# Performance work log

Hardware: AMD Instinct MI355X
Metric: run time of the kernel (lower is better)

The kernel has to match this reference:

```python
import jax, jax.numpy as jnp
import numpy as np

RADIUS = 0.2
NSAMPLE = 32
EPS = 1e-5  # BatchNorm2d default eps


def _bn_relu(x, g, b):
    # BatchNorm2d in training mode: per-channel stats over (B, S, nsample), biased var.
    m = x.mean(axis=(0, 1, 2))
    v = jnp.mean((x - m) ** 2, axis=(0, 1, 2))
    return jax.nn.relu((x - m) * jax.lax.rsqrt(v + EPS) * g + b)


def setup_inputs() -> dict:
    key = jax.random.key(0)
    ks = jax.random.split(key, 8)
    B, N, S = 8, 8192, 2048
    xyz = jax.random.uniform(ks[0], (B, 3, N), dtype=jnp.float32)          # unit cube
    points = jax.random.normal(ks[1], (B, 3, N), dtype=jnp.float32)
    fps_idx = jax.random.randint(ks[2], (B, S), 0, N, dtype=jnp.int32)
    W1 = jax.random.normal(ks[3], (64, 6), dtype=jnp.float32) * 0.1
    W2 = jax.random.normal(ks[4], (64, 64), dtype=jnp.float32) * 0.1
    W3 = jax.random.normal(ks[5], (128, 64), dtype=jnp.float32) * 0.1
    return dict(
        xyz=xyz, points=points, fps_idx=fps_idx,
        W1=W1, g1=jnp.ones((64,)), b1=jnp.zeros((64,)),
        W2=W2, g2=jnp.ones((64,)), b2=jnp.zeros((64,)),
        W3=W3, g3=jnp.ones((128,)), b3=jnp.zeros((128,)),
    )


def reference(xyz, points, fps_idx, W1, g1, b1, W2, g2, b2, W3, g3, b3):
    B, _, N = xyz.shape
    xyz_t = jnp.transpose(xyz, (0, 2, 1))            # [B,N,3]
    pts_t = jnp.transpose(points, (0, 2, 1))         # [B,N,D]
    # gather_operation: sampled centers
    new_xyz_t = jnp.take_along_axis(xyz_t, fps_idx[:, :, None], axis=1)  # [B,S,3]
    # ball query: first NSAMPLE points within radius; pad with first hit
    d2 = jnp.sum((new_xyz_t[:, :, None, :] - xyz_t[:, None, :, :]) ** 2, axis=-1)  # [B,S,N]
    keys = jnp.where(d2 <= RADIUS * RADIUS, jnp.arange(N, dtype=jnp.int32), N)
    neg_top, _ = jax.lax.top_k(-keys, NSAMPLE)       # smallest keys first
    idx = -neg_top                                   # [B,S,NSAMPLE]
    idx = jnp.where(idx < N, idx, idx[:, :, 0:1])    # pad empty slots with first hit (self always in-radius)
    bidx = jnp.arange(B)[:, None, None]
    grouped_xyz = xyz_t[bidx, idx]                   # [B,S,ns,3]
    rel = grouped_xyz - new_xyz_t[:, :, None, :]     # center-relative coords
    grouped_pts = pts_t[bidx, idx]                   # [B,S,ns,D]
    feat = jnp.concatenate([rel, grouped_pts], axis=-1)  # [B,S,ns,3+D]
    for W, g, b in ((W1, g1, b1), (W2, g2, b2), (W3, g3, b3)):
        feat = _bn_relu(jnp.einsum('bsnc,oc->bsno', feat, W), g, b)
    new_points = jnp.max(feat, axis=2)               # max over neighbors -> [B,S,C]
    return jnp.transpose(new_xyz_t, (0, 2, 1)), jnp.transpose(new_points, (0, 2, 1))
```

## Files before the change

### kernel.cpp

```cpp
#include <hip/hip_runtime.h>
#include <hip/hip_bf16.h>

#define BB_ 8
#define NN_ 8192
#define SS_ 2048
#define NS 32
#define C1 64
#define C2 64
#define C3 128
#define RAD2 0.04f
#define BN_EPS 1e-5f
#define M_TOT (BB_*SS_*NS)

typedef __attribute__((ext_vector_type(8))) short bf16x8;
typedef __attribute__((ext_vector_type(4))) float f32x4;

#define FBF_OFF 0
#define WPK_OFF 2097152
#define ST_OFF  2104320
#define AFF_OFF 2104832
#define GMM_OFF 2105344

__device__ inline unsigned pkbf(float a, float b) {
    __hip_bfloat162 h = __float22bfloat162_rn(make_float2(a, b));
    unsigned r; __builtin_memcpy(&r, &h, 4); return r;
}
__device__ inline bf16x8 asfrag(uint4 v) { bf16x8 r; __builtin_memcpy(&r, &v, 16); return r; }
__device__ inline float bflo(unsigned u) { unsigned x = u << 16; float f; __builtin_memcpy(&f, &x, 4); return f; }
__device__ inline float bfhi(unsigned u) { unsigned x = u & 0xffff0000u; float f; __builtin_memcpy(&f, &x, 4); return f; }

__global__ void k_zero(float* __restrict__ st) { st[threadIdx.x] = 0.f; }

__global__ void k_ballquery(const float* __restrict__ xyz, const float* __restrict__ pts,
                            const int* __restrict__ fps, uint4* __restrict__ fbf) {
    __shared__ int lidx[4][NS];
    int wave = (blockIdx.x * blockDim.x + threadIdx.x) >> 6;
    int lane = threadIdx.x & 63;
    int wslot = threadIdx.x >> 6;
    int b = wave / SS_;
    const float* xb = xyz + (size_t)b * 3 * NN_;
    const float* pb = pts + (size_t)b * 3 * NN_;
    int ci = fps[wave];
    float cx = xb[ci], cy = xb[NN_ + ci], cz = xb[2 * NN_ + ci];

    int found = 0;
    int first_i = -1;
    for (int base = 0; base < NN_; base += 64) {
        int i = base + lane;
        float dx = xb[i] - cx, dy = xb[NN_ + i] - cy, dz = xb[2 * NN_ + i] - cz;
        float d2 = __fadd_rn(__fadd_rn(__fmul_rn(dx, dx), __fmul_rn(dy, dy)), __fmul_rn(dz, dz));
        bool inr = d2 <= RAD2;
        unsigned long long mask = __ballot(inr);
        if (first_i < 0 && mask) first_i = base + __builtin_ctzll(mask);
        if (inr) {
            int pos = found + __popcll(mask & ((1ull << lane) - 1ull));
            if (pos < NS) lidx[wslot][pos] = i;
        }
        found += __popcll(mask);
        if (found >= NS) break;
    }
    if (found > NS) found = NS;
    __syncthreads();

    if (lane < NS) {
        int j = (lane < found) ? lidx[wslot][lane] : first_i;
        uint4 o;
        o.x = pkbf(xb[j] - cx,           xb[NN_ + j] - cy);
        o.y = pkbf(xb[2 * NN_ + j] - cz, pb[j]);
        o.z = pkbf(pb[NN_ + j],          pb[2 * NN_ + j]);
        o.w = 0u;
        fbf[(size_t)wave * NS + lane] = o;
    }
}

__global__ void k_xyz(const float* __restrict__ xyz, const int* __restrict__ fps,
                      float* __restrict__ out_xyz) {
    int t = blockIdx.x * 256 + threadIdx.x;
    if (t >= BB_ * 3 * SS_) return;
    int b = t / (3 * SS_);
    int r = (t / SS_) % 3;
    int s = t % SS_;
    int ci = fps[b * SS_ + s];
    out_xyz[t] = xyz[((size_t)b * 3 + r) * NN_ + ci];
}

__global__ void k_pack(const float* __restrict__ W1, const float* __restrict__ W2,
                       const float* __restrict__ W3, uint4* __restrict__ wf) {
    int t = blockIdx.x * 256 + threadIdx.x;
    if (t >= 1792) return;
    int l = t & 63, p = l & 15, qd = l >> 4;
    float v[8];
    if (t < 256) {
        int mt = t >> 6;
        #pragma unroll
        for (int j = 0; j < 8; ++j)
            v[j] = (qd == 0 && j < 6) ? W1[(mt * 16 + p) * 6 + j] : 0.f;
    } else if (t < 768) {
        int fr = (t - 256) >> 6;
        int mt = fr >> 1, kf = fr & 1;
        #pragma unroll
        for (int j = 0; j < 8; ++j)
            v[j] = W2[(16 * mt + p) * 64 + kf * 32 + qd * 8 + j];
    } else {
        int fr = (t - 768) >> 6;
        int nt = fr >> 1, kf = fr & 1;
        #pragma unroll
        for (int j = 0; j < 8; ++j)
            v[j] = W3[(nt * 16 + p) * 64 + kf * 32 + qd * 8 + j];
    }
    uint4 o;
    o.x = pkbf(v[0], v[1]); o.y = pkbf(v[2], v[3]);
    o.z = pkbf(v[4], v[5]); o.w = pkbf(v[6], v[7]);
    wf[t] = o;
}

__global__ void k_p1(const uint4* __restrict__ fbf, float* __restrict__ st) {
    __shared__ float sacc[27];
    int tid = threadIdx.x;
    if (tid < 27) sacc[tid] = 0.f;
    __syncthreads();
    int gt = blockIdx.x * 256 + tid;
    float vals[27];
    #pragma unroll
    for (int i = 0; i < 27; ++i) vals[i] = 0.f;
    #pragma unroll 1
    for (int it = 0; it < M_TOT / 16384; ++it) {
        uint4 w = fbf[it * 16384 + gt];
        float f[6] = { bflo(w.x), bfhi(w.x), bflo(w.y), bfhi(w.y), bflo(w.z), bfhi(w.z) };
        #pragma unroll
        for (int c = 0; c < 6; ++c) vals[c] += f[c];
        int q = 6;
        #pragma unroll
        for (int c = 0; c < 6; ++c)
            #pragma unroll
            for (int d = c; d < 6; ++d) { vals[q] = fmaf(f[c], f[d], vals[q]); ++q; }
    }
    int lane = tid & 63;
    #pragma unroll
    for (int i = 0; i < 27; ++i) {
        float v = vals[i];
        #pragma unroll
        for (int d = 32; d; d >>= 1) v += __shfl_xor(v, d);
        if (lane == 0) atomicAdd(&sacc[i], v);
    }
    __syncthreads();
    if (tid < 27) atomicAdd(&st[tid], sacc[tid]);
}

__global__ void k_fin1(const float* __restrict__ st, const float* __restrict__ W1,
                       const float* __restrict__ g, const float* __restrict__ bb,
                       float* __restrict__ a, float* __restrict__ c) {
    int o = threadIdx.x;
    if (o >= C1) return;
    float w[6];
    #pragma unroll
    for (int i = 0; i < 6; ++i) w[i] = W1[o * 6 + i];
    float ms = 0.f;
    #pragma unroll
    for (int i = 0; i < 6; ++i) ms = fmaf(w[i], st[i], ms);
    float m = ms / (float)M_TOT;
    float e2 = 0.f;
    #pragma unroll
    for (int ci = 0; ci < 6; ++ci)
        #pragma unroll
        for (int d = 0; d < 6; ++d) {
            int lo = ci < d ? ci : d, hi = ci < d ? d : ci;
            int idx = 6 + lo * 6 - lo * (lo + 1) / 2 + hi;
            e2 = fmaf(w[ci] * w[d], st[idx], e2);
        }
    float var = e2 / (float)M_TOT - m * m;
    float ai = g[o] * (1.0f / sqrtf(var + BN_EPS));
    a[o] = ai;
    c[o] = bb[o] - m * ai;
}

__global__ void k_fin(const float* __restrict__ gsum, const float* __restrict__ gsq,
                      const float* __restrict__ g, const float* __restrict__ bb,
                      float* __restrict__ a, float* __restrict__ c, int C) {
    int t = threadIdx.x;
    if (t < C) {
        float m = gsum[t] / (float)M_TOT;
        float var = gsq[t] / (float)M_TOT - m * m;
        float ai = g[t] * (1.0f / sqrtf(var + BN_EPS));
        a[t] = ai;
        c[t] = bb[t] - m * ai;
    }
}

__global__ __launch_bounds__(256) void k_p2(
        const uint4* __restrict__ fbf, const uint4* __restrict__ wpk,
        const float* __restrict__ aff,
        float* __restrict__ gsum, float* __restrict__ gsq) {
    __shared__ unsigned yls[4][2560];
    __shared__ float bs[C2], bq[C2];
    int tid = threadIdx.x, wslot = tid >> 6, lane = tid & 63;
    int p = lane & 15, qd = lane >> 4;
    if (tid < C2) { bs[tid] = 0.f; bq[tid] = 0.f; }
    __syncthreads();
    const float* a1 = aff, *c1 = aff + 64;
    const uint4* w1f = wpk;
    const uint4* w2f = wpk + 256;
    unsigned* my = yls[wslot];
    float s2[4][4], q2[4][4];
    #pragma unroll
    for (int i = 0; i < 4; ++i)
        #pragma unroll
        for (int r = 0; r < 4; ++r) { s2[i][r] = 0.f; q2[i][r] = 0.f; }

    #pragma unroll 1
    for (int it = 0; it < 4; ++it) {
        int tile = it * 2048 + blockIdx.x * 4 + wslot;
        int base = tile * 64;
        bf16x8 B1[4];
        #pragma unroll
        for (int nt = 0; nt < 4; ++nt) {
            uint4 v = make_uint4(0u, 0u, 0u, 0u);
            if (qd == 0) v = fbf[base + nt * 16 + p];
            B1[nt] = asfrag(v);
        }
        #pragma unroll
        for (int mt = 0; mt < 4; ++mt) {
            bf16x8 A = asfrag(w1f[mt * 64 + lane]);
            float4 av = *(const float4*)(a1 + mt * 16 + qd * 4);
            float4 cv = *(const float4*)(c1 + mt * 16 + qd * 4);
            #pragma unroll
            for (int nt = 0; nt < 4; ++nt) {
                f32x4 acc = {0.f, 0.f, 0.f, 0.f};
                acc = __builtin_amdgcn_mfma_f32_16x16x32_bf16(A, B1[nt], acc, 0, 0, 0);
                float y0 = fmaxf(fmaf(av.x, acc[0], cv.x), 0.f);
                float y1 = fmaxf(fmaf(av.y, acc[1], cv.y), 0.f);
                float y2 = fmaxf(fmaf(av.z, acc[2], cv.z), 0.f);
                float y3 = fmaxf(fmaf(av.w, acc[3], cv.w), 0.f);
                int a = (nt * 16 + p) * 40 + mt * 8 + qd * 2;
                *(uint2*)&my[a] = make_uint2(pkbf(y0, y1), pkbf(y2, y3));
            }
        }
        __syncthreads();
        bf16x8 B2[4][2];
        #pragma unroll
        for (int nt = 0; nt < 4; ++nt)
            #pragma unroll
            for (int kf = 0; kf < 2; ++kf)
                B2[nt][kf] = asfrag(*(const uint4*)&my[(nt * 16 + p) * 40 + kf * 16 + qd * 4]);
        #pragma unroll
        for (int mt = 0; mt < 4; ++mt) {
            f32x4 acc[4];
            #pragma unroll
            for (int nt = 0; nt < 4; ++nt) acc[nt] = (f32x4){0.f, 0.f, 0.f, 0.f};
            #pragma unroll
            for (int kf = 0; kf < 2; ++kf) {
                bf16x8 W = asfrag(w2f[(mt * 2 + kf) * 64 + lane]);
                #pragma unroll
                for (int nt = 0; nt < 4; ++nt)
                    acc[nt] = __builtin_amdgcn_mfma_f32_16x16x32_bf16(W, B2[nt][kf], acc[nt], 0, 0, 0);
            }
            #pragma unroll
            for (int r = 0; r < 4; ++r) {
                float v0 = acc[0][r], v1 = acc[1][r], v2 = acc[2][r], v3 = acc[3][r];
                s2[mt][r] += (v0 + v1) + (v2 + v3);
                q2[mt][r] = fmaf(v0, v0, fmaf(v1, v1, fmaf(v2, v2, fmaf(v3, v3, q2[mt][r]))));
            }
        }
        __syncthreads();
    }
    #pragma unroll
    for (int mt = 0; mt < 4; ++mt)
        #pragma unroll
        for (int r = 0; r < 4; ++r) {
            float s = s2[mt][r], q = q2[mt][r];
            #pragma unroll
            for (int off = 1; off <= 8; off <<= 1) { s += __shfl_xor(s, off); q += __shfl_xor(q, off); }
            if (p == 0) {
                atomicAdd(&bs[mt * 16 + qd * 4 + r], s);
                atomicAdd(&bq[mt * 16 + qd * 4 + r], q);
            }
        }
    __syncthreads();
    if (tid < C2) { atomicAdd(&gsum[tid], bs[tid]); atomicAdd(&gsq[tid], bq[tid]); }
}

__global__ __launch_bounds__(256) void k_p3(
        const uint4* __restrict__ fbf, const uint4* __restrict__ wpk,
        const float* __restrict__ aff,
        float* __restrict__ gsum, float* __restrict__ gsq, float2* __restrict__ gmm) {
    __shared__ unsigned yls[4][2560];
    __shared__ float bs[C3], bq[C3];
    int tid = threadIdx.x, wslot = tid >> 6, lane = tid & 63;
    int p = lane & 15, qd = lane >> 4;
    if (tid < 128) bs[tid] = 0.f; else bq[tid - 128] = 0.f;
    __syncthreads();
    const float* a1 = aff, *c1 = aff + 64, *a2 = aff + 128, *c2 = aff + 192;
    const uint4* w1f = wpk;
    const uint4* w2f = wpk + 256;
    const uint4* w3f = wpk + 768;
    unsigned* my = yls[wslot];
    bf16x8 W3f[8][2];
    #pragma unroll
    for (int nt = 0; nt < 8; ++nt)
        #pragma unroll
        for (int kf = 0; kf < 2; ++kf)
            W3f[nt][kf] = asfrag(w3f[(nt * 2 + kf) * 64 + lane]);
    float gs3[8], gq3[8];
    #pragma unroll
    for (int i = 0; i < 8; ++i) { gs3[i] = 0.f; gq3[i] = 0.f; }

    #pragma unroll 1
    for (int it = 0; it < 4; ++it) {
        int tile = it * 2048 + blockIdx.x * 4 + wslot;
        int base = tile * 64;
        bf16x8 B1[4];
        #pragma unroll
        for (int nt = 0; nt < 4; ++nt) {
            uint4 v = make_uint4(0u, 0u, 0u, 0u);
            if (qd == 0) v = fbf[base + nt * 16 + p];
            B1[nt] = asfrag(v);
        }
        #pragma unroll
        for (int mt = 0; mt < 4; ++mt) {
            bf16x8 A = asfrag(w1f[mt * 64 + lane]);
            float4 av = *(const float4*)(a1 + mt * 16 + qd * 4);
            float4 cv = *(const float4*)(c1 + mt * 16 + qd * 4);
            #pragma unroll
            for (int nt = 0; nt < 4; ++nt) {
                f32x4 acc = {0.f, 0.f, 0.f, 0.f};
                acc = __builtin_amdgcn_mfma_f32_16x16x32_bf16(A, B1[nt], acc, 0, 0, 0);
                float y0 = fmaxf(fmaf(av.x, acc[0], cv.x), 0.f);
                float y1 = fmaxf(fmaf(av.y, acc[1], cv.y), 0.f);
                float y2 = fmaxf(fmaf(av.z, acc[2], cv.z), 0.f);
                float y3 = fmaxf(fmaf(av.w, acc[3], cv.w), 0.f);
                int a = (nt * 16 + p) * 40 + mt * 8 + qd * 2;
                *(uint2*)&my[a] = make_uint2(pkbf(y0, y1), pkbf(y2, y3));
            }
        }
        __syncthreads();
        bf16x8 B2[4][2];
        #pragma unroll
        for (int nt = 0; nt < 4; ++nt)
            #pragma unroll
            for (int kf = 0; kf < 2; ++kf)
                B2[nt][kf] = asfrag(*(const uint4*)&my[(nt * 16 + p) * 40 + kf * 16 + qd * 4]);
        __syncthreads();
        #pragma unroll
        for (int mt = 0; mt < 4; ++mt) {
            f32x4 acc[4];
            #pragma unroll
            for (int nt = 0; nt < 4; ++nt) acc[nt] = (f32x4){0.f, 0.f, 0.f, 0.f};
            #pragma unroll
            for (int kf = 0; kf < 2; ++kf) {
                bf16x8 W = asfrag(w2f[(mt * 2 + kf) * 64 + lane]);
                #pragma unroll
                for (int nt = 0; nt < 4; ++nt)
                    acc[nt] = __builtin_amdgcn_mfma_f32_16x16x32_bf16(W, B2[nt][kf], acc[nt], 0, 0, 0);
            }
            float4 av = *(const float4*)(a2 + mt * 16 + qd * 4);
            float4 cv = *(const float4*)(c2 + mt * 16 + qd * 4);
            #pragma unroll
            for (int nt = 0; nt < 4; ++nt) {
                float y0 = fmaxf(fmaf(av.x, acc[nt][0], cv.x), 0.f);
                float y1 = fmaxf(fmaf(av.y, acc[nt][1], cv.y), 0.f);
                float y2 = fmaxf(fmaf(av.z, acc[nt][2], cv.z), 0.f);
                float y3 = fmaxf(fmaf(av.w, acc[nt][3], cv.w), 0.f);
                int a = (nt * 16 + p) * 40 + mt * 8 + qd * 2;
                *(uint2*)&my[a] = make_uint2(pkbf(y0, y1), pkbf(y2, y3));
            }
        }
        __syncthreads();
        float gmx[2][8], gmn[2][8];
        #pragma unroll
        for (int mt = 0; mt < 4; ++mt) {
            bf16x8 A0 = asfrag(*(const uint4*)&my[(mt * 16 + p) * 40 + qd * 4]);
            bf16x8 A1 = asfrag(*(const uint4*)&my[(mt * 16 + p) * 40 + 16 + qd * 4]);
            f32x4 acc[8];
            #pragma unroll
            for (int nt = 0; nt < 8; ++nt) {
                acc[nt] = __builtin_amdgcn_mfma_f32_16x16x32_bf16(A0, W3f[nt][0],
                            (f32x4){0.f, 0.f, 0.f, 0.f}, 0, 0, 0);
                acc[nt] = __builtin_amdgcn_mfma_f32_16x16x32_bf16(A1, W3f[nt][1], acc[nt], 0, 0, 0);
            }
            int gh = mt >> 1;
            #pragma unroll
            for (int nt = 0; nt < 8; ++nt) {
                float v0 = acc[nt][0], v1 = acc[nt][1], v2 = acc[nt][2], v3 = acc[nt][3];
                gs3[nt] += (v0 + v1) + (v2 + v3);
                gq3[nt] = fmaf(v0, v0, fmaf(v1, v1, fmaf(v2, v2, fmaf(v3, v3, gq3[nt]))));
                float mx = fmaxf(fmaxf(v0, v1), fmaxf(v2, v3));
                float mn = fminf(fminf(v0, v1), fminf(v2, v3));
                if ((mt & 1) == 0) { gmx[gh][nt] = mx; gmn[gh][nt] = mn; }
                else { gmx[gh][nt] = fmaxf(gmx[gh][nt], mx); gmn[gh][nt] = fminf(gmn[gh][nt], mn); }
            }
        }
        #pragma unroll
        for (int grp = 0; grp < 2; ++grp)
            #pragma unroll
            for (int nt = 0; nt < 8; ++nt) {
                float mx = gmx[grp][nt], mn = gmn[grp][nt];
                mx = fmaxf(mx, __shfl_xor(mx, 16)); mx = fmaxf(mx, __shfl_xor(mx, 32));
                mn = fminf(mn, __shfl_xor(mn, 16)); mn = fminf(mn, __shfl_xor(mn, 32));
                if (lane < 16)
                    gmm[(size_t)(tile * 2 + grp) * C3 + nt * 16 + lane] = make_float2(mx, mn);
            }
        __syncthreads();
    }
    #pragma unroll
    for (int nt = 0; nt < 8; ++nt) {
        float s = gs3[nt], q = gq3[nt];
        s += __shfl_xor(s, 16); s += __shfl_xor(s, 32);
        q += __shfl_xor(q, 16); q += __shfl_xor(q, 32);
        if (lane < 16) {
            atomicAdd(&bs[nt * 16 + lane], s);
            atomicAdd(&bq[nt * 16 + lane], q);
        }
    }
    __syncthreads();
    if (tid < C3) { atomicAdd(&gsum[tid], bs[tid]); atomicAdd(&gsq[tid], bq[tid]); }
}

__global__ void k_out(const float2* __restrict__ gmm, const float* __restrict__ a3,
                      const float* __restrict__ c3, float* __restrict__ outp) {
    int s = blockIdx.x * 256 + threadIdx.x;
    int o = blockIdx.y, b = blockIdx.z;
    float2 mm = gmm[((size_t)(b * SS_ + s)) * C3 + o];
    float a = a3[o], c = c3[o];
    float v = (a >= 0.f) ? mm.x : mm.y;
    outp[((size_t)b * C3 + o) * SS_ + s] = fmaxf(fmaf(a, v, c), 0.f);
}

extern "C" void kernel_launch(void* const* d_in, const int* in_sizes, int n_in,
                              void* d_out, int out_size, void* d_ws, size_t ws_size,
                              hipStream_t stream) {
    (void)in_sizes; (void)n_in; (void)out_size; (void)ws_size;
    const float* xyz = (const float*)d_in[0];
    const float* pts = (const float*)d_in[1];
    const int*   fps = (const int*)d_in[2];
    const float* W1 = (const float*)d_in[3];
    const float* g1 = (const float*)d_in[4];
    const float* b1 = (const float*)d_in[5];
    const float* W2 = (const float*)d_in[6];
    const float* g2 = (const float*)d_in[7];
    const float* b2 = (const float*)d_in[8];
    const float* W3 = (const float*)d_in[9];
    const float* g3 = (const float*)d_in[10];
    const float* b3 = (const float*)d_in[11];
    float* out = (float*)d_out;
    float* ws = (float*)d_ws;

    uint4* fbf = (uint4*)(ws + FBF_OFF);
    uint4* wpk = (uint4*)(ws + WPK_OFF);
    float* st  = ws + ST_OFF;
    float* sum2 = st + 64,  *sq2 = st + 128;
    float* sum3 = st + 192, *sq3 = st + 320;
    float* af = ws + AFF_OFF;
    float* a1 = af,       *c1 = af + 64;
    float* a2 = af + 128, *c2 = af + 192;
    float* a3 = af + 256, *c3 = af + 384;
    float2* gmm = (float2*)(ws + GMM_OFF);

    k_zero<<<1, 512, 0, stream>>>(st);
    k_pack<<<7, 256, 0, stream>>>(W1, W2, W3, wpk);
    k_ballquery<<<(BB_ * SS_) / 4, 256, 0, stream>>>(xyz, pts, fps, fbf);
    k_p1<<<64, 256, 0, stream>>>(fbf, st);
    k_fin1<<<1, 64, 0, stream>>>(st, W1, g1, b1, a1, c1);
    k_p2<<<512, 256, 0, stream>>>(fbf, wpk, af, sum2, sq2);
    k_fin<<<1, 128, 0, stream>>>(sum2, sq2, g2, b2, a2, c2, C2);
    k_p3<<<512, 256, 0, stream>>>(fbf, wpk, af, sum3, sq3, gmm);
    k_fin<<<1, 128, 0, stream>>>(sum3, sq3, g3, b3, a3, c3, C3);
    k_out<<<dim3(SS_ / 256, C3, BB_), 256, 0, stream>>>(gmm, a3, c3,
                                                        out + (size_t)BB_ * 3 * SS_);
    k_xyz<<<(BB_ * 3 * SS_ + 255) / 256, 256, 0, stream>>>(xyz, fps, out);
}
```

Before: 247.5 us.

## Merge small kernels, stage W3 in LDS, store single max, coalesce output

Folds the stats zeroing into the weight-pack kernel and the xyz gather into a new output kernel that transposes through shared memory for coalesced float4 stores. The conv kernels now use doubled grids with launch_bounds occupancy hints, a YSTR=34 LDS row stride, and wave-local fences in place of block barriers. Layer 3 keeps W3 in LDS instead of registers and picks max or negated min by the sign of g3 inside the kernel, storing one float per channel instead of a max/min pair. The aim is fewer launches, less register pressure, less global traffic and fewer LDS bank conflicts. The risks are extra LDS reads for W3 and reliance on wave-private LDS buffers for correctness.

```diff
diff --git a/kernel.cpp b/kernel.cpp
--- a/kernel.cpp
+++ b/kernel.cpp
@@ -11,6 +11,7 @@
 #define RAD2 0.04f
 #define BN_EPS 1e-5f
 #define M_TOT (BB_*SS_*NS)
+#define YSTR 34
 
 typedef __attribute__((ext_vector_type(8))) short bf16x8;
 typedef __attribute__((ext_vector_type(4))) float f32x4;
@@ -28,8 +29,6 @@
 __device__ inline bf16x8 asfrag(uint4 v) { bf16x8 r; __builtin_memcpy(&r, &v, 16); return r; }
 __device__ inline float bflo(unsigned u) { unsigned x = u << 16; float f; __builtin_memcpy(&f, &x, 4); return f; }
 __device__ inline float bfhi(unsigned u) { unsigned x = u & 0xffff0000u; float f; __builtin_memcpy(&f, &x, 4); return f; }
-
-__global__ void k_zero(float* __restrict__ st) { st[threadIdx.x] = 0.f; }
 
 __global__ void k_ballquery(const float* __restrict__ xyz, const float* __restrict__ pts,
                             const int* __restrict__ fps, uint4* __restrict__ fbf) {
@@ -73,21 +72,11 @@
     }
 }
 
-__global__ void k_xyz(const float* __restrict__ xyz, const int* __restrict__ fps,
-                      float* __restrict__ out_xyz) {
+__global__ void k_pack(const float* __restrict__ W1, const float* __restrict__ W2,
+                       const float* __restrict__ W3, uint4* __restrict__ wf,
+                       float* __restrict__ st) {
+    if (blockIdx.x == 7) { st[threadIdx.x] = 0.f; st[threadIdx.x + 256] = 0.f; return; }
     int t = blockIdx.x * 256 + threadIdx.x;
-    if (t >= BB_ * 3 * SS_) return;
-    int b = t / (3 * SS_);
-    int r = (t / SS_) % 3;
-    int s = t % SS_;
-    int ci = fps[b * SS_ + s];
-    out_xyz[t] = xyz[((size_t)b * 3 + r) * NN_ + ci];
-}
-
-__global__ void k_pack(const float* __restrict__ W1, const float* __restrict__ W2,
-                       const float* __restrict__ W3, uint4* __restrict__ wf) {
-    int t = blockIdx.x * 256 + threadIdx.x;
-    if (t >= 1792) return;
     int l = t & 63, p = l & 15, qd = l >> 4;
     float v[8];
     if (t < 256) {
@@ -124,8 +113,8 @@
     #pragma unroll
     for (int i = 0; i < 27; ++i) vals[i] = 0.f;
     #pragma unroll 1
-    for (int it = 0; it < M_TOT / 16384; ++it) {
-        uint4 w = fbf[it * 16384 + gt];
+    for (int it = 0; it < M_TOT / 65536; ++it) {
+        uint4 w = fbf[it * 65536 + gt];
         float f[6] = { bflo(w.x), bfhi(w.x), bflo(w.y), bfhi(w.y), bflo(w.z), bfhi(w.z) };
         #pragma unroll
         for (int c = 0; c < 6; ++c) vals[c] += f[c];
@@ -187,11 +176,11 @@
     }
 }
 
-__global__ __launch_bounds__(256) void k_p2(
+__global__ __launch_bounds__(256, 4) void k_p2(
         const uint4* __restrict__ fbf, const uint4* __restrict__ wpk,
         const float* __restrict__ aff,
         float* __restrict__ gsum, float* __restrict__ gsq) {
-    __shared__ unsigned yls[4][2560];
+    __shared__ unsigned yls[4][64 * YSTR];
     __shared__ float bs[C2], bq[C2];
     int tid = threadIdx.x, wslot = tid >> 6, lane = tid & 63;
     int p = lane & 15, qd = lane >> 4;
@@ -208,8 +197,8 @@
         for (int r = 0; r < 4; ++r) { s2[i][r] = 0.f; q2[i][r] = 0.f; }
 
     #pragma unroll 1
-    for (int it = 0; it < 4; ++it) {
-        int tile = it * 2048 + blockIdx.x * 4 + wslot;
+    for (int it = 0; it < 2; ++it) {
+        int tile = it * 4096 + blockIdx.x * 4 + wslot;
         int base = tile * 64;
         bf16x8 B1[4];
         #pragma unroll
@@ -231,17 +220,17 @@
                 float y1 = fmaxf(fmaf(av.y, acc[1], cv.y), 0.f);
                 float y2 = fmaxf(fmaf(av.z, acc[2], cv.z), 0.f);
                 float y3 = fmaxf(fmaf(av.w, acc[3], cv.w), 0.f);
-                int a = (nt * 16 + p) * 40 + mt * 8 + qd * 2;
+                int a = (nt * 16 + p) * YSTR + mt * 8 + qd * 2;
                 *(uint2*)&my[a] = make_uint2(pkbf(y0, y1), pkbf(y2, y3));
             }
         }
-        __syncthreads();
+        __threadfence_block();
         bf16x8 B2[4][2];
         #pragma unroll
         for (int nt = 0; nt < 4; ++nt)
             #pragma unroll
             for (int kf = 0; kf < 2; ++kf)
-                B2[nt][kf] = asfrag(*(const uint4*)&my[(nt * 16 + p) * 40 + kf * 16 + qd * 4]);
+                B2[nt][kf] = asfrag(*(const uint4*)&my[(nt * 16 + p) * YSTR + kf * 16 + qd * 4]);
         #pragma unroll
         for (int mt = 0; mt < 4; ++mt) {
             f32x4 acc[4];
@@ -261,7 +250,7 @@
                 q2[mt][r] = fmaf(v0, v0, fmaf(v1, v1, fmaf(v2, v2, fmaf(v3, v3, q2[mt][r]))));
             }
         }
-        __syncthreads();
+        __threadfence_block();
     }
     #pragma unroll
     for (int mt = 0; mt < 4; ++mt)
@@ -279,34 +268,31 @@
     if (tid < C2) { atomicAdd(&gsum[tid], bs[tid]); atomicAdd(&gsq[tid], bq[tid]); }
 }
 
-__global__ __launch_bounds__(256) void k_p3(
+__global__ __launch_bounds__(256, 3) void k_p3(
         const uint4* __restrict__ fbf, const uint4* __restrict__ wpk,
-        const float* __restrict__ aff,
-        float* __restrict__ gsum, float* __restrict__ gsq, float2* __restrict__ gmm) {
-    __shared__ unsigned yls[4][2560];
+        const float* __restrict__ aff, const float* __restrict__ g3,
+        float* __restrict__ gsum, float* __restrict__ gsq, float* __restrict__ gmm) {
+    __shared__ unsigned yls[4][64 * YSTR];
+    __shared__ uint4 w3ls[1024];
     __shared__ float bs[C3], bq[C3];
     int tid = threadIdx.x, wslot = tid >> 6, lane = tid & 63;
     int p = lane & 15, qd = lane >> 4;
     if (tid < 128) bs[tid] = 0.f; else bq[tid - 128] = 0.f;
+    #pragma unroll
+    for (int i = 0; i < 4; ++i) w3ls[i * 256 + tid] = wpk[768 + i * 256 + tid];
     __syncthreads();
     const float* a1 = aff, *c1 = aff + 64, *a2 = aff + 128, *c2 = aff + 192;
     const uint4* w1f = wpk;
     const uint4* w2f = wpk + 256;
-    const uint4* w3f = wpk + 768;
     unsigned* my = yls[wslot];
-    bf16x8 W3f[8][2];
-    #pragma unroll
-    for (int nt = 0; nt < 8; ++nt)
-        #pragma unroll
-        for (int kf = 0; kf < 2; ++kf)
-            W3f[nt][kf] = asfrag(w3f[(nt * 2 + kf) * 64 + lane]);
     float gs3[8], gq3[8];
-    #pragma unroll
-    for (int i = 0; i < 8; ++i) { gs3[i] = 0.f; gq3[i] = 0.f; }
+    bool pos[8];
+    #pragma unroll
+    for (int i = 0; i < 8; ++i) { gs3[i] = 0.f; gq3[i] = 0.f; pos[i] = g3[i * 16 + p] >= 0.f; }
 
     #pragma unroll 1
-    for (int it = 0; it < 4; ++it) {
-        int tile = it * 2048 + blockIdx.x * 4 + wslot;
+    for (int it = 0; it < 2; ++it) {
+        int tile = it * 4096 + blockIdx.x * 4 + wslot;
         int base = tile * 64;
         bf16x8 B1[4];
         #pragma unroll
@@ -328,18 +314,18 @@
                 float y1 = fmaxf(fmaf(av.y, acc[1], cv.y), 0.f);
                 float y2 = fmaxf(fmaf(av.z, acc[2], cv.z), 0.f);
                 float y3 = fmaxf(fmaf(av.w, acc[3], cv.w), 0.f);
-                int a = (nt * 16 + p) * 40 + mt * 8 + qd * 2;
+                int a = (nt * 16 + p) * YSTR + mt * 8 + qd * 2;
                 *(uint2*)&my[a] = make_uint2(pkbf(y0, y1), pkbf(y2, y3));
             }
         }
-        __syncthreads();
+        __threadfence_block();
         bf16x8 B2[4][2];
         #pragma unroll
         for (int nt = 0; nt < 4; ++nt)
             #pragma unroll
             for (int kf = 0; kf < 2; ++kf)
-                B2[nt][kf] = asfrag(*(const uint4*)&my[(nt * 16 + p) * 40 + kf * 16 + qd * 4]);
-        __syncthreads();
+                B2[nt][kf] = asfrag(*(const uint4*)&my[(nt * 16 + p) * YSTR + kf * 16 + qd * 4]);
+        __threadfence_block();
         #pragma unroll
         for (int mt = 0; mt < 4; ++mt) {
             f32x4 acc[4];
@@ -360,46 +346,51 @@
                 float y1 = fmaxf(fmaf(av.y, acc[nt][1], cv.y), 0.f);
                 float y2 = fmaxf(fmaf(av.z, acc[nt][2], cv.z), 0.f);
                 float y3 = fmaxf(fmaf(av.w, acc[nt][3], cv.w), 0.f);
-                int a = (nt * 16 + p) * 40 + mt * 8 + qd * 2;
+                int a = (nt * 16 + p) * YSTR + mt * 8 + qd * 2;
                 *(uint2*)&my[a] = make_uint2(pkbf(y0, y1), pkbf(y2, y3));
             }
         }
-        __syncthreads();
-        float gmx[2][8], gmn[2][8];
+        __threadfence_block();
+        bf16x8 A3[4][2];
         #pragma unroll
         for (int mt = 0; mt < 4; ++mt) {
-            bf16x8 A0 = asfrag(*(const uint4*)&my[(mt * 16 + p) * 40 + qd * 4]);
-            bf16x8 A1 = asfrag(*(const uint4*)&my[(mt * 16 + p) * 40 + 16 + qd * 4]);
-            f32x4 acc[8];
-            #pragma unroll
-            for (int nt = 0; nt < 8; ++nt) {
-                acc[nt] = __builtin_amdgcn_mfma_f32_16x16x32_bf16(A0, W3f[nt][0],
+            A3[mt][0] = asfrag(*(const uint4*)&my[(mt * 16 + p) * YSTR + qd * 4]);
+            A3[mt][1] = asfrag(*(const uint4*)&my[(mt * 16 + p) * YSTR + 16 + qd * 4]);
+        }
+        __threadfence_block();
+        #pragma unroll
+        for (int nt = 0; nt < 8; ++nt) {
+            bf16x8 Wa = asfrag(w3ls[(nt * 2 + 0) * 64 + lane]);
+            bf16x8 Wb = asfrag(w3ls[(nt * 2 + 1) * 64 + lane]);
+            f32x4 acc[4];
+            #pragma unroll
+            for (int mt = 0; mt < 4; ++mt) {
+                acc[mt] = __builtin_amdgcn_mfma_f32_16x16x32_bf16(A3[mt][0], Wa,
                             (f32x4){0.f, 0.f, 0.f, 0.f}, 0, 0, 0);
-                acc[nt] = __builtin_amdgcn_mfma_f32_16x16x32_bf16(A1, W3f[nt][1], acc[nt], 0, 0, 0);
-            }
-            int gh = mt >> 1;
-            #pragma unroll
-            for (int nt = 0; nt < 8; ++nt) {
-                float v0 = acc[nt][0], v1 = acc[nt][1], v2 = acc[nt][2], v3 = acc[nt][3];
-                gs3[nt] += (v0 + v1) + (v2 + v3);
-                gq3[nt] = fmaf(v0, v0, fmaf(v1, v1, fmaf(v2, v2, fmaf(v3, v3, gq3[nt]))));
+                acc[mt] = __builtin_amdgcn_mfma_f32_16x16x32_bf16(A3[mt][1], Wb, acc[mt], 0, 0, 0);
+            }
+            float s = 0.f, q = 0.f, va = 0.f, vb = 0.f;
+            #pragma unroll
+            for (int mt = 0; mt < 4; ++mt) {
+                float v0 = acc[mt][0], v1 = acc[mt][1], v2 = acc[mt][2], v3 = acc[mt][3];
+                s += (v0 + v1) + (v2 + v3);
+                q = fmaf(v0, v0, fmaf(v1, v1, fmaf(v2, v2, fmaf(v3, v3, q))));
                 float mx = fmaxf(fmaxf(v0, v1), fmaxf(v2, v3));
                 float mn = fminf(fminf(v0, v1), fminf(v2, v3));
-                if ((mt & 1) == 0) { gmx[gh][nt] = mx; gmn[gh][nt] = mn; }
-                else { gmx[gh][nt] = fmaxf(gmx[gh][nt], mx); gmn[gh][nt] = fminf(gmn[gh][nt], mn); }
-            }
-        }
-        #pragma unroll
-        for (int grp = 0; grp < 2; ++grp)
-            #pragma unroll
-            for (int nt = 0; nt < 8; ++nt) {
-                float mx = gmx[grp][nt], mn = gmn[grp][nt];
-                mx = fmaxf(mx, __shfl_xor(mx, 16)); mx = fmaxf(mx, __shfl_xor(mx, 32));
-                mn = fminf(mn, __shfl_xor(mn, 16)); mn = fminf(mn, __shfl_xor(mn, 32));
-                if (lane < 16)
-                    gmm[(size_t)(tile * 2 + grp) * C3 + nt * 16 + lane] = make_float2(mx, mn);
-            }
-        __syncthreads();
+                float vv = pos[nt] ? mx : -mn;
+                if (mt == 0) va = vv;
+                else if (mt == 1) va = fmaxf(va, vv);
+                else if (mt == 2) vb = vv;
+                else vb = fmaxf(vb, vv);
+            }
+            gs3[nt] += s; gq3[nt] += q;
+            va = fmaxf(va, __shfl_xor(va, 16)); va = fmaxf(va, __shfl_xor(va, 32));
+            vb = fmaxf(vb, __shfl_xor(vb, 16)); vb = fmaxf(vb, __shfl_xor(vb, 32));
+            if (lane < 16) {
+                gmm[(size_t)(tile * 2 + 0) * C3 + nt * 16 + lane] = va;
+                gmm[(size_t)(tile * 2 + 1) * C3 + nt * 16 + lane] = vb;
+            }
+        }
     }
     #pragma unroll
     for (int nt = 0; nt < 8; ++nt) {
@@ -415,14 +406,41 @@
     if (tid < C3) { atomicAdd(&gsum[tid], bs[tid]); atomicAdd(&gsq[tid], bq[tid]); }
 }
 
-__global__ void k_out(const float2* __restrict__ gmm, const float* __restrict__ a3,
-                      const float* __restrict__ c3, float* __restrict__ outp) {
-    int s = blockIdx.x * 256 + threadIdx.x;
-    int o = blockIdx.y, b = blockIdx.z;
-    float2 mm = gmm[((size_t)(b * SS_ + s)) * C3 + o];
-    float a = a3[o], c = c3[o];
-    float v = (a >= 0.f) ? mm.x : mm.y;
-    outp[((size_t)b * C3 + o) * SS_ + s] = fmaxf(fmaf(a, v, c), 0.f);
+__global__ void k_outx(const float* __restrict__ gmm, const float* __restrict__ af,
+                       const float* __restrict__ xyz, const int* __restrict__ fps,
+                       float* __restrict__ out) {
+    __shared__ float T[C3][17];
+    int blk = blockIdx.x, tid = threadIdx.x;
+    if (blk < 1024) {
+        const float* a3 = af + 256;
+        const float* c3 = af + 384;
+        int b = blk >> 7, s0 = (blk & 127) << 4;
+        #pragma unroll
+        for (int i = 0; i < 8; ++i) {
+            int idx = i * 256 + tid;
+            int sl = idx >> 7, o = idx & 127;
+            float m = gmm[((size_t)(b * SS_ + s0 + sl)) * C3 + o];
+            float a = a3[o];
+            float v = (a >= 0.f) ? m : -m;
+            T[o][sl] = fmaxf(fmaf(a, v, c3[o]), 0.f);
+        }
+        __syncthreads();
+        int o = tid & 127, sh = tid >> 7;
+        float* dst = out + (size_t)BB_ * 3 * SS_ + ((size_t)b * C3 + o) * SS_ + s0 + sh * 8;
+        float4 w0, w1;
+        w0.x = T[o][sh * 8 + 0]; w0.y = T[o][sh * 8 + 1];
+        w0.z = T[o][sh * 8 + 2]; w0.w = T[o][sh * 8 + 3];
+        w1.x = T[o][sh * 8 + 4]; w1.y = T[o][sh * 8 + 5];
+        w1.z = T[o][sh * 8 + 6]; w1.w = T[o][sh * 8 + 7];
+        *(float4*)dst = w0; *(float4*)(dst + 4) = w1;
+    } else {
+        int t = (blk - 1024) * 256 + tid;
+        int b = t / (3 * SS_);
+        int r = (t / SS_) % 3;
+        int s = t % SS_;
+        int ci = fps[b * SS_ + s];
+        out[t] = xyz[((size_t)b * 3 + r) * NN_ + ci];
+    }
 }
 
 extern "C" void kernel_launch(void* const* d_in, const int* in_sizes, int n_in,
@@ -453,18 +471,15 @@
     float* a1 = af,       *c1 = af + 64;
     float* a2 = af + 128, *c2 = af + 192;
     float* a3 = af + 256, *c3 = af + 384;
-    float2* gmm = (float2*)(ws + GMM_OFF);
-
-    k_zero<<<1, 512, 0, stream>>>(st);
-    k_pack<<<7, 256, 0, stream>>>(W1, W2, W3, wpk);
+    float* gmm = ws + GMM_OFF;
+
+    k_pack<<<8, 256, 0, stream>>>(W1, W2, W3, wpk, st);
     k_ballquery<<<(BB_ * SS_) / 4, 256, 0, stream>>>(xyz, pts, fps, fbf);
-    k_p1<<<64, 256, 0, stream>>>(fbf, st);
+    k_p1<<<256, 256, 0, stream>>>(fbf, st);
     k_fin1<<<1, 64, 0, stream>>>(st, W1, g1, b1, a1, c1);
-    k_p2<<<512, 256, 0, stream>>>(fbf, wpk, af, sum2, sq2);
+    k_p2<<<1024, 256, 0, stream>>>(fbf, wpk, af, sum2, sq2);
     k_fin<<<1, 128, 0, stream>>>(sum2, sq2, g2, b2, a2, c2, C2);
-    k_p3<<<512, 256, 0, stream>>>(fbf, wpk, af, sum3, sq3, gmm);
+    k_p3<<<1024, 256, 0, stream>>>(fbf, wpk, af, g3, sum3, sq3, gmm);
     k_fin<<<1, 128, 0, stream>>>(sum3, sq3, g3, b3, a3, c3, C3);
-    k_out<<<dim3(SS_ / 256, C3, BB_), 256, 0, stream>>>(gmm, a3, c3,
-                                                        out + (size_t)BB_ * 3 * SS_);
-    k_xyz<<<(BB_ * 3 * SS_ + 255) / 256, 256, 0, stream>>>(xyz, fps, out);
-}
+    k_outx<<<1024 + 192, 256, 0, stream>>>(gmm, af, xyz, fps, out);
+}
```

After: 322.7 us. 1.3x slower.
